# Performance work log

Measured on AMD Instinct MI355X. Metric: run time of the kernel, lower is better.

Reference implementation:

```python
import jax, jax.numpy as jnp
import numpy as np

B, H, W = 16, 512, 512
N_BINS = 511          # round(mean(shape)) - 1 for (512, 512)
MAX_R = 1.0           # (1 + min(shape)/max(shape)) / 2 for square image


def _bin_ids():
    # Precompute per-pixel radial shell index (replaces the list of boolean shell masks).
    frame = max(H, W)
    xx, yy = np.mgrid[:H, :W]
    ellipse = ((xx - H / 2) * 2 / frame) ** 2 + ((yy - W / 2) * 2 / frame) ** 2
    r2 = np.linspace(0.0, MAX_R, N_BINS + 1)[1:] ** 2
    # shell k = { r2[k-1] <= ellipse < r2[k] }; pixels with ellipse >= r2[-1] map to
    # overflow bin N_BINS and are dropped, exactly matching the xor'd ellipse masks.
    return jnp.asarray(np.searchsorted(r2, ellipse.ravel(), side='right').astype(np.int32))


BIN_IDS = _bin_ids()  # [H*W] int32 in [0, N_BINS]


def setup_inputs() -> dict:
    key = jax.random.key(0)
    k1, k2 = jax.random.split(key)
    return {
        "z_": jax.random.normal(k1, (B, H, W, 2), dtype=jnp.float32),
        "t_": jax.random.normal(k2, (B, H, W, 2), dtype=jnp.float32),
    }


def _shell_sums(x):
    # x: [B, H*W] -> per-shell sums [B, N_BINS+1] in a single fused segment-sum pass.
    return jax.vmap(lambda v: jax.ops.segment_sum(v, BIN_IDS, num_segments=N_BINS + 1))(x)


def reference(z_, t_):
    tc = t_[..., 0] + 1j * t_[..., 1]          # [B,H,W] complex target
    zc = z_[..., 0] + 1j * z_[..., 1]
    Ft = jnp.fft.fft2(tc, axes=(-2, -1))
    Fe = jnp.fft.fft2(zc - tc, axes=(-2, -1))
    norm_coeff = Ft.real ** 2 + Ft.imag ** 2   # |FFT(target)|^2, [B,H,W]
    errors = Fe.real ** 2 + Fe.imag ** 2       # |FFT(z - target)|^2
    es = _shell_sums(errors.reshape(B, -1))[:, :N_BINS]      # drop overflow bin
    ns = _shell_sums(norm_coeff.reshape(B, -1))[:, :N_BINS]
    nre = es / jnp.maximum(ns, 1e-8)           # per-batch, per-shell normed error
    # per_shell_loss = per-batch sum over shells; loss = mean over batch
    return jnp.mean(jnp.sum(nre, axis=1))
```

## Files before the change

### kernel.cpp

```cpp
#include <hip/hip_runtime.h>

#define HH 512
#define WW 512
#define NBATCH 16
#define NBINS 512

#define PI_F 3.14159265358979323846f

#define SW(r) ((r) ^ (((r) >> 4) & 0xF))
#define TSW(c, hh) (((c) << 3) + ((hh) ^ (((c) >> 1) & 7)))

__device__ __forceinline__ float2 cadd(float2 a, float2 b){ return make_float2(a.x+b.x, a.y+b.y); }
__device__ __forceinline__ float2 csub(float2 a, float2 b){ return make_float2(a.x-b.x, a.y-b.y); }
__device__ __forceinline__ float2 cmul(float2 a, float2 b){
    return make_float2(a.x*b.x - a.y*b.y, a.x*b.y + a.y*b.x);
}

__device__ __forceinline__ void dft8(const float2* a, float2* y) {
    const float s2 = 0.70710678118654752440f;
    float2 t02a = cadd(a[0], a[4]), t02s = csub(a[0], a[4]);
    float2 t13a = cadd(a[2], a[6]), t13s = csub(a[2], a[6]);
    float2 E0 = cadd(t02a, t13a);
    float2 E2 = csub(t02a, t13a);
    float2 E1 = make_float2(t02s.x + t13s.y, t02s.y - t13s.x);
    float2 E3 = make_float2(t02s.x - t13s.y, t02s.y + t13s.x);
    float2 u02a = cadd(a[1], a[5]), u02s = csub(a[1], a[5]);
    float2 u13a = cadd(a[3], a[7]), u13s = csub(a[3], a[7]);
    float2 O0 = cadd(u02a, u13a);
    float2 O2 = csub(u02a, u13a);
    float2 O1 = make_float2(u02s.x + u13s.y, u02s.y - u13s.x);
    float2 O3 = make_float2(u02s.x - u13s.y, u02s.y + u13s.x);
    float2 wO1 = make_float2(s2 * (O1.x + O1.y), s2 * (O1.y - O1.x));
    float2 wO2 = make_float2(O2.y, -O2.x);
    float2 wO3 = make_float2(s2 * (O3.y - O3.x), -s2 * (O3.x + O3.y));
    y[0] = cadd(E0, O0);  y[4] = csub(E0, O0);
    y[1] = cadd(E1, wO1); y[5] = csub(E1, wO1);
    y[2] = cadd(E2, wO2); y[6] = csub(E2, wO2);
    y[3] = cadd(E3, wO3); y[7] = csub(E3, wO3);
}

__device__ __forceinline__ void twiddle8(float base, float2* w) {
    float s1, c1, s4, c4;
    __sincosf(base, &s1, &c1);
    __sincosf(4.0f * base, &s4, &c4);
    w[0] = make_float2(1.0f, 0.0f);
    w[1] = make_float2(c1, s1);
    w[2] = cmul(w[1], w[1]);
    w[3] = cmul(w[2], w[1]);
    w[4] = make_float2(c4, s4);
    w[5] = cmul(w[4], w[1]);
    w[6] = cmul(w[4], w[2]);
    w[7] = cmul(w[4], w[3]);
}

__device__ __forceinline__ void fft512_stage0_store(float2* rb, int lane, const float2* a) {
    float2 y[8]; dft8(a, y);
    float2 w[8]; twiddle8(-PI_F * (float)lane * (1.0f / 256.0f), w);
#pragma unroll
    for (int r = 0; r < 8; ++r) rb[SW(8 * lane + r)] = cmul(y[r], w[r]);
}

__device__ __forceinline__ void fft512_stage1(float2* rb, int lane) {
    float2 a[8];
#pragma unroll
    for (int u = 0; u < 8; ++u) a[u] = rb[SW(lane + 64 * u)];
    float2 y[8]; dft8(a, y);
    float2 w[8]; twiddle8(-PI_F * (float)(lane >> 3) * (1.0f / 32.0f), w);
    const int qb = (lane & 7) + ((lane >> 3) << 6);
#pragma unroll
    for (int r = 0; r < 8; ++r) rb[SW(qb + 8 * r)] = cmul(y[r], w[r]);
}

__device__ __forceinline__ void fft512_stage2(const float2* rb, int lane, float2* y) {
    float2 a[8];
#pragma unroll
    for (int u = 0; u < 8; ++u) a[u] = rb[SW(lane + 64 * u)];
    dft8(a, y);
}

__global__ __launch_bounds__(512, 4)
void row_fft_kernel(const float2* __restrict__ z, const float2* __restrict__ t,
                    float2* __restrict__ fieldsT, int b0) {
    __shared__ float2 buf[8 * 512];
    const int tid  = threadIdx.x;
    const int lane = tid & 63;
    const int g    = tid >> 6;
    const int bid  = blockIdx.x;
    const int hg   = bid & 63;
    const int lb   = bid >> 6;
    const int b    = b0 + lb;
    const int h    = (hg << 3) | g;
    const size_t rowOff = ((size_t)(b * HH + h)) * WW;

    const float2* tr = t + rowOff;
    const float2* zr = z + rowOff;
    float2 tv[8], zv[8];
#pragma unroll
    for (int u = 0; u < 8; ++u) tv[u] = tr[lane + 64 * u];
#pragma unroll
    for (int u = 0; u < 8; ++u) zv[u] = zr[lane + 64 * u];

    float2* rb = buf + (g << 9);
#pragma unroll
    for (int f = 0; f < 2; ++f) {
        float2 a[8];
        if (f == 0) {
#pragma unroll
            for (int u = 0; u < 8; ++u) a[u] = tv[u];
        } else {
#pragma unroll
            for (int u = 0; u < 8; ++u) a[u] = make_float2(zv[u].x - tv[u].x,
                                                           zv[u].y - tv[u].y);
        }
        fft512_stage0_store(rb, lane, a);
        __builtin_amdgcn_wave_barrier();
        fft512_stage1(rb, lane);
        __builtin_amdgcn_wave_barrier();
        float2 y[8];
        fft512_stage2(rb, lane, y);

        __syncthreads();
#pragma unroll
        for (int r = 0; r < 8; ++r) {
            int c = lane + (r << 6);
            buf[TSW(c, g)] = y[r];
        }
        __syncthreads();
        float2* outF = fieldsT + ((size_t)(lb * 2 + f) << 18);
#pragma unroll
        for (int k = 0; k < 8; ++k) {
            int e  = tid + (k << 9);
            int c  = e >> 3;
            int hh = e & 7;
            outF[((size_t)c << 9) + (hg << 3) + hh] = buf[TSW(c, hh)];
        }
        __syncthreads();
    }
}

__global__ __launch_bounds__(512, 4)
void col_fft_bin_kernel(const float2* __restrict__ fieldsT,
                        float* __restrict__ partials, int b0) {
    __shared__ float2 buf[8 * 512];
    const int tid  = threadIdx.x;
    const int lane = tid & 63;
    const int g    = tid >> 6;
    const int bid  = blockIdx.x;
    const int cg   = bid & 63;
    const int fl   = bid >> 6;
    const int f    = fl & 1;
    const int b    = b0 + (fl >> 1);
    const int c    = (cg << 3) | g;

    const float2* colT = fieldsT + (((size_t)fl << 9) + c) * 512;
    float2 a[8];
#pragma unroll
    for (int u = 0; u < 8; ++u) a[u] = colT[lane + (u << 6)];

    float2* rb = buf + (g << 9);
    fft512_stage0_store(rb, lane, a);
    __builtin_amdgcn_wave_barrier();
    fft512_stage1(rb, lane);
    __builtin_amdgcn_wave_barrier();
    float2 y[8];
    fft512_stage2(rb, lane, y);
    __builtin_amdgcn_wave_barrier();
    __asm__ volatile("" ::: "memory");

#pragma unroll
    for (int j = 0; j < 4; ++j) rb[lane + (j << 6)] = make_float2(0.0f, 0.0f);
    __builtin_amdgcn_wave_barrier();
    __asm__ volatile("" ::: "memory");

    float* histw = (float*)rb;
    const int dc = c - 256;
    const unsigned fc2i = (unsigned)(dc * dc);
#pragma unroll
    for (int r = 0; r < 8; ++r) {
        int k  = lane + (r << 6);
        int dk = k - 256;
        unsigned m = (unsigned)(dk * dk) + fc2i;
        if (m < 65536u) {
            int bin = (int)(sqrtf((float)m) * (511.0f / 256.0f));
            unsigned long long rhs = 261121ull * (unsigned long long)m;
            unsigned bp1 = (unsigned)(bin + 1);
            if (((unsigned long long)(bp1 * bp1) << 16) <= rhs) ++bin;
            else if (((unsigned long long)((unsigned)bin * (unsigned)bin) << 16) > rhs) --bin;
            atomicAdd(&histw[bin], y[r].x * y[r].x + y[r].y * y[r].y);
        }
    }
    __syncthreads();

    float s = 0.0f;
    const float* bufF = (const float*)buf;
#pragma unroll
    for (int gg = 0; gg < 8; ++gg) s += bufF[(gg << 10) + tid];
    partials[(((size_t)cg << 5) + (size_t)(f * NBATCH + b)) * NBINS + tid] = s;
}

__global__ __launch_bounds__(512)
void reduce_bins_kernel(const float* __restrict__ partials, float* __restrict__ bins) {
    __shared__ float red[512];
    const int tid = threadIdx.x;
    const int fl  = blockIdx.x >> 2;
    const int q   = blockIdx.x & 3;
    const int bin = (q << 7) + (tid & 127);
    const int ch  = tid >> 7;
    float s = 0.0f;
#pragma unroll
    for (int j = 0; j < 16; ++j) {
        int cg = (ch << 4) + j;
        s += partials[((size_t)(cg << 5) + fl) * NBINS + bin];
    }
    red[tid] = s;
    __syncthreads();
    if (tid < 128) {
        bins[(size_t)fl * NBINS + bin] =
            red[tid] + red[tid + 128] + red[tid + 256] + red[tid + 384];
    }
}

__global__ __launch_bounds__(512)
void loss_kernel(const float* __restrict__ bins, float* __restrict__ outp) {
    __shared__ float red[512];
    const int tid = threadIdx.x;
    float acc = 0.0f;
    if (tid < 511) {
#pragma unroll 4
        for (int b = 0; b < NBATCH; ++b) {
            float ns = bins[((size_t)b) * NBINS + tid];
            float es = bins[((size_t)(NBATCH + b)) * NBINS + tid];
            acc += es / fmaxf(ns, 1e-8f);
        }
    }
    red[tid] = acc;
    __syncthreads();
    for (int s = 256; s > 0; s >>= 1) {
        if (tid < s) red[tid] += red[tid + s];
        __syncthreads();
    }
    if (tid == 0) outp[0] = red[0] * (1.0f / NBATCH);
}

extern "C" void kernel_launch(void* const* d_in, const int* in_sizes, int n_in,
                              void* d_out, int out_size, void* d_ws, size_t ws_size,
                              hipStream_t stream) {
    const float2* z = (const float2*)d_in[0];
    const float2* t = (const float2*)d_in[1];
    float* outp = (float*)d_out;

    const size_t partialsBytes = 64ull * 2 * NBATCH * NBINS * sizeof(float);
    const size_t binsBytes     = (size_t)2 * NBATCH * NBINS * sizeof(float);
    const size_t fixedBytes    = partialsBytes + binsBytes;
    const size_t fpb = (size_t)2 * HH * WW * sizeof(float2);

    int CB = 16;
    while (CB > 1 && fixedBytes + (size_t)CB * fpb > ws_size) CB >>= 1;

    float*  partials = (float*)d_ws;
    float*  bins     = (float*)((char*)d_ws + partialsBytes);
    float2* fieldsT  = (float2*)((char*)d_ws + fixedBytes);

    for (int b0 = 0; b0 < NBATCH; b0 += CB) {
        row_fft_kernel<<<CB * 64, 512, 0, stream>>>(z, t, fieldsT, b0);
        col_fft_bin_kernel<<<CB * 2 * 64, 512, 0, stream>>>(fieldsT, partials, b0);
    }
    reduce_bins_kernel<<<128, 512, 0, stream>>>(partials, bins);
    loss_kernel<<<1, 512, 0, stream>>>(bins, outp);
}
```

Before: 161.3 us.

## Process both fields per column block and pre-reduce bin atomics with DPP

Each column-FFT block now transforms both fields (error and target) for the same column, with the second column's global loads issued before the first FFT's shared-memory stages. That halves the grid and reuses the bin computation for both fields. Same-bin contributions are combined across 16-lane rows with DPP segmented scans before one LDS atomic per run, aimed at reducing atomic contention. The cost is higher register pressure and fewer blocks for latency hiding. Out-of-range pixels are routed to overflow bin 511 instead of being skipped.

```diff
diff --git a/kernel.cpp b/kernel.cpp
--- a/kernel.cpp
+++ b/kernel.cpp
@@ -9,6 +9,9 @@
 
 #define SW(r) ((r) ^ (((r) >> 4) & 0xF))
 #define TSW(c, hh) (((c) << 3) + ((hh) ^ (((c) >> 1) & 7)))
+
+#define DPP_SHR(x, n) __builtin_amdgcn_update_dpp(0, (x), 0x110 + (n), 0xF, 0xF, true)
+#define DPP_SHL1(x)   __builtin_amdgcn_update_dpp(0, (x), 0x101,       0xF, 0xF, true)
 
 __device__ __forceinline__ float2 cadd(float2 a, float2 b){ return make_float2(a.x+b.x, a.y+b.y); }
 __device__ __forceinline__ float2 csub(float2 a, float2 b){ return make_float2(a.x-b.x, a.y-b.y); }
@@ -147,55 +150,97 @@
     const int g    = tid >> 6;
     const int bid  = blockIdx.x;
     const int cg   = bid & 63;
-    const int fl   = bid >> 6;
-    const int f    = fl & 1;
-    const int b    = b0 + (fl >> 1);
+    const int lb   = bid >> 6;
+    const int b    = b0 + lb;
     const int c    = (cg << 3) | g;
 
-    const float2* colT = fieldsT + (((size_t)fl << 9) + c) * 512;
+    const float2* colA = fieldsT + (((size_t)(lb * 2 + 0) << 9) + c) * 512;
+    const float2* colB = fieldsT + (((size_t)(lb * 2 + 1) << 9) + c) * 512;
+
+    float2* rb = buf + (g << 9);
+
     float2 a[8];
 #pragma unroll
-    for (int u = 0; u < 8; ++u) a[u] = colT[lane + (u << 6)];
-
-    float2* rb = buf + (g << 9);
+    for (int u = 0; u < 8; ++u) a[u] = colA[lane + (u << 6)];
     fft512_stage0_store(rb, lane, a);
+    float2 bB[8];
+#pragma unroll
+    for (int u = 0; u < 8; ++u) bB[u] = colB[lane + (u << 6)];
     __builtin_amdgcn_wave_barrier();
     fft512_stage1(rb, lane);
     __builtin_amdgcn_wave_barrier();
     float2 y[8];
     fft512_stage2(rb, lane, y);
+    float pA[8];
+#pragma unroll
+    for (int r = 0; r < 8; ++r) pA[r] = y[r].x * y[r].x + y[r].y * y[r].y;
     __builtin_amdgcn_wave_barrier();
     __asm__ volatile("" ::: "memory");
 
-#pragma unroll
-    for (int j = 0; j < 4; ++j) rb[lane + (j << 6)] = make_float2(0.0f, 0.0f);
+    fft512_stage0_store(rb, lane, bB);
+    __builtin_amdgcn_wave_barrier();
+    fft512_stage1(rb, lane);
+    __builtin_amdgcn_wave_barrier();
+    fft512_stage2(rb, lane, y);
     __builtin_amdgcn_wave_barrier();
     __asm__ volatile("" ::: "memory");
 
-    float* histw = (float*)rb;
+#pragma unroll
+    for (int j = 0; j < 8; ++j) rb[lane + (j << 6)] = make_float2(0.0f, 0.0f);
+    __builtin_amdgcn_wave_barrier();
+    __asm__ volatile("" ::: "memory");
+
+    float* histA = (float*)rb;
+    float* histB = histA + 512;
     const int dc = c - 256;
     const unsigned fc2i = (unsigned)(dc * dc);
+    const int l15 = lane & 15;
 #pragma unroll
     for (int r = 0; r < 8; ++r) {
         int k  = lane + (r << 6);
         int dk = k - 256;
         unsigned m = (unsigned)(dk * dk) + fc2i;
-        if (m < 65536u) {
-            int bin = (int)(sqrtf((float)m) * (511.0f / 256.0f));
-            unsigned long long rhs = 261121ull * (unsigned long long)m;
-            unsigned bp1 = (unsigned)(bin + 1);
-            if (((unsigned long long)(bp1 * bp1) << 16) <= rhs) ++bin;
-            else if (((unsigned long long)((unsigned)bin * (unsigned)bin) << 16) > rhs) --bin;
-            atomicAdd(&histw[bin], y[r].x * y[r].x + y[r].y * y[r].y);
+        int bin = (int)(sqrtf((float)m) * (511.0f / 256.0f));
+        unsigned long long rhs = 261121ull * (unsigned long long)m;
+        unsigned bp1 = (unsigned)(bin + 1);
+        if (((unsigned long long)(bp1 * bp1) << 16) <= rhs) ++bin;
+        else if (((unsigned long long)((unsigned)bin * (unsigned)bin) << 16) > rhs) --bin;
+        bin = (m < 65536u) ? bin : 511;
+
+        float v = pA[r];
+        float w = y[r].x * y[r].x + y[r].y * y[r].y;
+
+        int nb; bool take;
+        nb = DPP_SHR(bin, 1); take = (l15 >= 1 && nb == bin);
+        v += take ? __int_as_float(DPP_SHR(__float_as_int(v), 1)) : 0.0f;
+        w += take ? __int_as_float(DPP_SHR(__float_as_int(w), 1)) : 0.0f;
+        nb = DPP_SHR(bin, 2); take = (l15 >= 2 && nb == bin);
+        v += take ? __int_as_float(DPP_SHR(__float_as_int(v), 2)) : 0.0f;
+        w += take ? __int_as_float(DPP_SHR(__float_as_int(w), 2)) : 0.0f;
+        nb = DPP_SHR(bin, 4); take = (l15 >= 4 && nb == bin);
+        v += take ? __int_as_float(DPP_SHR(__float_as_int(v), 4)) : 0.0f;
+        w += take ? __int_as_float(DPP_SHR(__float_as_int(w), 4)) : 0.0f;
+        nb = DPP_SHR(bin, 8); take = (l15 >= 8 && nb == bin);
+        v += take ? __int_as_float(DPP_SHR(__float_as_int(v), 8)) : 0.0f;
+        w += take ? __int_as_float(DPP_SHR(__float_as_int(w), 8)) : 0.0f;
+
+        int nxt = DPP_SHL1(bin);
+        if (l15 == 15 || nxt != bin) {
+            atomicAdd(&histA[bin], v);
+            atomicAdd(&histB[bin], w);
         }
     }
     __syncthreads();
 
-    float s = 0.0f;
     const float* bufF = (const float*)buf;
-#pragma unroll
-    for (int gg = 0; gg < 8; ++gg) s += bufF[(gg << 10) + tid];
-    partials[(((size_t)cg << 5) + (size_t)(f * NBATCH + b)) * NBINS + tid] = s;
+    float sA = 0.0f, sB = 0.0f;
+#pragma unroll
+    for (int gg = 0; gg < 8; ++gg) {
+        sA += bufF[(gg << 10) + tid];
+        sB += bufF[(gg << 10) + 512 + tid];
+    }
+    partials[(((size_t)cg << 5) + (size_t)b) * NBINS + tid] = sA;
+    partials[(((size_t)cg << 5) + (size_t)(NBATCH + b)) * NBINS + tid] = sB;
 }
 
 __global__ __launch_bounds__(512)
@@ -263,7 +308,7 @@
 
     for (int b0 = 0; b0 < NBATCH; b0 += CB) {
         row_fft_kernel<<<CB * 64, 512, 0, stream>>>(z, t, fieldsT, b0);
-        col_fft_bin_kernel<<<CB * 2 * 64, 512, 0, stream>>>(fieldsT, partials, b0);
+        col_fft_bin_kernel<<<CB * 64, 512, 0, stream>>>(fieldsT, partials, b0);
     }
     reduce_bins_kernel<<<128, 512, 0, stream>>>(partials, bins);
     loss_kernel<<<1, 512, 0, stream>>>(bins, outp);
```

After: 160.8 us. Within noise of the previous version (-0.3%).
